# Kernel tuning notes

Measured on AMD Instinct MI355X. Metric: run time of the kernel, lower is better.

## Reference

```python
import jax, jax.numpy as jnp
import numpy as np

B, D_IN, HD, HN = 16384, 1024, 128, 8
D = HD * HN  # 1024
PROJ = int((4.0 / 3.0) * D)  # 1365
EPS = 1e-5


def setup_inputs() -> dict:
    key = jax.random.key(0)
    ks = jax.random.split(key, 16)
    s = 0.02
    inp = {
        'seq': jax.random.normal(ks[0], (B, D_IN), jnp.float32),
        'c0': jnp.zeros((B, D), jnp.float32),
        'n0': jnp.ones((B, D), jnp.float32),
        'h0': jax.random.normal(ks[1], (B, D), jnp.float32) * 0.1,
        'm0': jnp.zeros((B, D), jnp.float32),
        'ln_w': jnp.ones((D_IN,), jnp.float32),
        'ln_b': jnp.zeros((D_IN,), jnp.float32),
        'Wz': jax.random.normal(ks[2], (D, D_IN), jnp.float32) * s,
        'bz': jnp.zeros((D,), jnp.float32),
        'Wi': jax.random.normal(ks[3], (D, D_IN), jnp.float32) * s,
        'bi': jnp.zeros((D,), jnp.float32),
        'Wo': jax.random.normal(ks[4], (D, D_IN), jnp.float32) * s,
        'bo': jnp.zeros((D,), jnp.float32),
        'Wf': jax.random.normal(ks[5], (D, D_IN), jnp.float32) * s,
        'bf': jnp.zeros((D,), jnp.float32),
        'Rz': jax.random.normal(ks[6], (HN, HD, HD), jnp.float32) * s,
        'Ri': jax.random.normal(ks[7], (HN, HD, HD), jnp.float32) * s,
        'Ro': jax.random.normal(ks[8], (HN, HD, HD), jnp.float32) * s,
        'Rf': jax.random.normal(ks[9], (HN, HD, HD), jnp.float32) * s,
        'gn_w': jnp.ones((D,), jnp.float32),
        'gn_b': jnp.zeros((D,), jnp.float32),
        'up_w': jax.random.normal(ks[10], (2 * PROJ, D), jnp.float32) * s,
        'up_b': jnp.zeros((2 * PROJ,), jnp.float32),
        'down_w': jax.random.normal(ks[11], (D_IN, PROJ), jnp.float32) * s,
        'down_b': jnp.zeros((D_IN,), jnp.float32),
    }
    return inp


def _layernorm(x, w, b):
    mu = jnp.mean(x, axis=-1, keepdims=True)
    var = jnp.mean(jnp.square(x - mu), axis=-1, keepdims=True)
    return (x - mu) * jax.lax.rsqrt(var + EPS) * w + b


def _groupnorm(x, w, b):
    # x: (B, D) -> groups of HD channels per head
    xr = x.reshape(x.shape[0], HN, HD)
    mu = jnp.mean(xr, axis=-1, keepdims=True)
    var = jnp.mean(jnp.square(xr - mu), axis=-1, keepdims=True)
    xn = ((xr - mu) * jax.lax.rsqrt(var + EPS)).reshape(x.shape)
    return xn * w + b


def _block_linear(h, R):
    # block-diagonal recurrence: per-head (HD,HD) matmul
    hr = h.reshape(h.shape[0], HN, HD)
    return jnp.einsum('hed,bhd->bhe', R, hr).reshape(h.shape)


def reference(seq, c0, n0, h0, m0, ln_w, ln_b, Wz, bz, Wi, bi, Wo, bo, Wf, bf,
              Rz, Ri, Ro, Rf, gn_w, gn_b, up_w, up_b, down_w, down_b):
    x_t = _layernorm(seq, ln_w, ln_b)
    x_c = x_t  # use_conv=False default path
    i_t = x_c @ Wi.T + bi + _block_linear(h0, Ri)
    f_t = x_c @ Wf.T + bf + _block_linear(h0, Rf)
    z_t = x_t @ Wz.T + bz + _block_linear(h0, Rz)
    o_t = x_t @ Wo.T + bo + _block_linear(h0, Ro)
    m_t = jnp.maximum(f_t + m0, i_t)
    i_e = jnp.exp(i_t - m_t)
    f_e = jnp.exp(f_t - m_t + m0)
    z_a = jnp.tanh(z_t)
    o_a = jax.nn.sigmoid(o_t)
    c_t = f_e * c0 + i_e * z_a
    n_t = f_e * n0 + i_e
    h_t = o_a * (c_t / n_t)
    out = _groupnorm(h_t, gn_w, gn_b)
    up = out @ up_w.T + up_b
    out1, out2 = jnp.split(up, 2, axis=-1)
    out = out1 + jax.nn.gelu(out2, approximate=False)
    out = out @ down_w.T + down_b
    return (out + seq, c_t, n_t, h_t, m_t)
```

## Files before the change

kernel.cpp:

```cpp
#include <hip/hip_runtime.h>
#include <hip/hip_bf16.h>
#include <cstdint>
#include <type_traits>

typedef __attribute__((ext_vector_type(8))) __bf16 bf16x8;
typedef __attribute__((ext_vector_type(8))) short short8;
typedef __attribute__((ext_vector_type(4))) float f32x4;
using u16 = unsigned short;

template <typename T, typename = void> struct mfma_ok : std::false_type {};
template <typename T>
struct mfma_ok<T, std::void_t<decltype(__builtin_amdgcn_mfma_f32_16x16x32_bf16(
    std::declval<T>(), std::declval<T>(), std::declval<f32x4>(), 0, 0, 0))>>
    : std::true_type {};
using frag_t = std::conditional_t<mfma_ok<bf16x8>::value, bf16x8, short8>;
static_assert(sizeof(frag_t) == 16, "frag must be 4 VGPRs");

template <typename T>
__device__ __forceinline__ f32x4 MFMA(T a, T b, f32x4 c) {
  return __builtin_amdgcn_mfma_f32_16x16x32_bf16(a, b, c, 0, 0, 0);
}

__device__ __forceinline__ void gl_lds16(const u16* g, u16* l) {
  __builtin_amdgcn_global_load_lds(
      (const __attribute__((address_space(1))) unsigned int*)g,
      (__attribute__((address_space(3))) unsigned int*)l, 16, 0, 0);
}

__device__ __forceinline__ u16 f2bf(float v) {
  __hip_bfloat16 h = __float2bfloat16(v);
  return __builtin_bit_cast(u16, h);
}

__device__ __forceinline__ int xcd_swz(int wid, int nwg) {
  return (wid & 7) * (nwg >> 3) + (wid >> 3);
}

__device__ __forceinline__ void gemm256(
    const u16* __restrict__ A, int lda,
    const u16* __restrict__ B, int ldb, int K,
    u16* lds, f32x4 (&acc)[8][4])
{
  const int t = threadIdx.x;
  const int l = t & 63;
  const int w = t >> 6;
  const int wm = w >> 2, wc = w & 3;

  const int cs = (t & 3) ^ ((t >> 3) & 3);
  const u16* gA = A + (t >> 2) * lda + cs * 8;
  const u16* gB = B + (t >> 2) * ldb + cs * 8;

  const int lr = l & 15, lk = l >> 4;
  const int ck = (lk ^ ((lr >> 1) & 3)) * 8;
  const int ab = (wm * 128 + lr) * 32 + ck;
  const int bb = 8192 + (wc * 64 + lr) * 32 + ck;

  const int ns = K >> 5;

#define STG(s) do {                                            \
    u16* s_ = lds + ((s) & 3) * 16384;                         \
    const u16* a_ = gA + (s) * 32;                             \
    const u16* b_ = gB + (s) * 32;                             \
    gl_lds16(a_,             s_ + w * 512);                    \
    gl_lds16(a_ + 128 * lda, s_ +  4096 + w * 512);            \
    gl_lds16(b_,             s_ +  8192 + w * 512);            \
    gl_lds16(b_ + 128 * ldb, s_ + 12288 + w * 512);            \
  } while (0)

  STG(0);
  STG(1);
  asm volatile("s_waitcnt vmcnt(4)" ::: "memory");
  __builtin_amdgcn_s_barrier();

  for (int s = 0; s < ns; ++s) {
    u16* cur = lds + (s & 3) * 16384;
    if (s + 2 < ns) STG(s + 2);

    frag_t a[8], b[4];
#pragma unroll
    for (int fm = 0; fm < 8; ++fm)
      a[fm] = *(const frag_t*)(cur + ab + fm * 512);
#pragma unroll
    for (int fn = 0; fn < 4; ++fn)
      b[fn] = *(const frag_t*)(cur + bb + fn * 512);

    __builtin_amdgcn_s_setprio(1);
#pragma unroll
    for (int fn = 0; fn < 4; ++fn)
#pragma unroll
      for (int fm = 0; fm < 8; ++fm)
        acc[fm][fn] = MFMA(a[fm], b[fn], acc[fm][fn]);
    __builtin_amdgcn_s_setprio(0);

    if (s + 1 < ns) {
      if (s + 2 < ns) asm volatile("s_waitcnt vmcnt(4)" ::: "memory");
      else            asm volatile("s_waitcnt vmcnt(0)" ::: "memory");
      __builtin_amdgcn_s_barrier();
    }
  }
#undef STG
}

__global__ __launch_bounds__(256) void prep_kernel(
    const float* __restrict__ Wi, const float* __restrict__ Wf,
    const float* __restrict__ Wz, const float* __restrict__ Wo,
    const float* __restrict__ Ri, const float* __restrict__ Rf,
    const float* __restrict__ Rz, const float* __restrict__ Ro,
    const float* __restrict__ upw, const float* __restrict__ dnw,
    u16* __restrict__ Wint, u16* __restrict__ Rint,
    u16* __restrict__ upint, u16* __restrict__ dnp)
{
  const int stride = gridDim.x * 256;
  for (int i = blockIdx.x * 256 + threadIdx.x; i < 9043968; i += stride) {
    if (i < 4194304) {
      const int s = i >> 18, v = (i >> 10) & 255, k = i & 1023;
      const int wc = v >> 6, gsel = (v >> 4) & 3, c16 = v & 15;
      const int srcRow = s * 64 + wc * 16 + c16;
      const float* W = (gsel == 0) ? Wi : (gsel == 1) ? Wf : (gsel == 2) ? Wz : Wo;
      Wint[i] = f2bf(W[srcRow * 1024 + k]);
    } else if (i < 4718592) {
      const int j = i - 4194304;
      const int s = j >> 15, v = (j >> 7) & 255, k = j & 127;
      const int wc = v >> 6, gsel = (v >> 4) & 3, c16 = v & 15;
      const int head = s >> 1;
      const int colInHead = (s & 1) * 64 + wc * 16 + c16;
      const float* R = (gsel == 0) ? Ri : (gsel == 1) ? Rf : (gsel == 2) ? Rz : Ro;
      Rint[j] = f2bf(R[head * 16384 + colInHead * 128 + k]);
    } else if (i < 7602176) {
      const int j = i - 4718592;
      const int vcol = j >> 10, k = j & 1023;
      const int tile = vcol >> 8, wc = (vcol >> 6) & 3;
      const int half = (vcol >> 5) & 1, c32 = vcol & 31;
      const int a = tile * 128 + wc * 32 + c32;
      upint[j] = (a < 1365) ? f2bf(upw[(half * 1365 + a) * 1024 + k]) : (u16)0;
    } else {
      const int j = i - 7602176;
      const int row = j / 1408, k = j - row * 1408;
      dnp[j] = (k < 1365) ? f2bf(dnw[row * 1365 + k]) : (u16)0;
    }
  }
}

__global__ __launch_bounds__(256) void ln_kernel(
    const float* __restrict__ seq, const float* __restrict__ h0,
    const float* __restrict__ lnw, const float* __restrict__ lnb,
    u16* __restrict__ xb, u16* __restrict__ h0b)
{
  const int row = blockIdx.x;
  const int t = threadIdx.x;
  const float4 v = ((const float4*)(seq + (size_t)row * 1024))[t];
  float s = v.x + v.y + v.z + v.w;
  float q = v.x * v.x + v.y * v.y + v.z * v.z + v.w * v.w;
#pragma unroll
  for (int o = 32; o >= 1; o >>= 1) { s += __shfl_xor(s, o); q += __shfl_xor(q, o); }
  __shared__ float sm[8];
  const int l = t & 63, w = t >> 6;
  if (l == 0) { sm[w] = s; sm[4 + w] = q; }
  __syncthreads();
  s = sm[0] + sm[1] + sm[2] + sm[3];
  q = sm[4] + sm[5] + sm[6] + sm[7];
  const float mu = s * (1.f / 1024.f);
  const float var = q * (1.f / 1024.f) - mu * mu;
  const float rstd = rsqrtf(var + 1e-5f);
  const float4 wv = ((const float4*)lnw)[t];
  const float4 bv = ((const float4*)lnb)[t];
  ushort4 o4;
  o4.x = f2bf((v.x - mu) * rstd * wv.x + bv.x);
  o4.y = f2bf((v.y - mu) * rstd * wv.y + bv.y);
  o4.z = f2bf((v.z - mu) * rstd * wv.z + bv.z);
  o4.w = f2bf((v.w - mu) * rstd * wv.w + bv.w);
  ((ushort4*)(xb + (size_t)row * 1024))[t] = o4;
  const float4 h = ((const float4*)(h0 + (size_t)row * 1024))[t];
  ushort4 h4;
  h4.x = f2bf(h.x); h4.y = f2bf(h.y); h4.z = f2bf(h.z); h4.w = f2bf(h.w);
  ((ushort4*)(h0b + (size_t)row * 1024))[t] = h4;
}

__global__ __launch_bounds__(512, 1) void gate_kernel(
    const u16* __restrict__ xb, const u16* __restrict__ h0b,
    const u16* __restrict__ Wint, const u16* __restrict__ Rint,
    const float* __restrict__ bi, const float* __restrict__ bfv,
    const float* __restrict__ bz, const float* __restrict__ bo,
    const float* __restrict__ c0, const float* __restrict__ n0i,
    const float* __restrict__ m0,
    float* __restrict__ oc, float* __restrict__ on,
    float* __restrict__ oh, float* __restrict__ om)
{
  __shared__ __align__(16) u16 lds[65536];
  const int wid = xcd_swz(blockIdx.x, 1024);
  const int s = wid & 15;
  const int m0r = (wid >> 4) * 256;
  f32x4 acc[8][4] = {};
  gemm256(xb + (size_t)m0r * 1024, 1024, Wint + s * 262144, 1024, 1024, lds, acc);
  const int head = s >> 1;
  gemm256(h0b + (size_t)m0r * 1024 + head * 128, 1024,
          Rint + s * 32768, 128, 128, lds, acc);

  const int t = threadIdx.x, l = t & 63, w = t >> 6, wm = w >> 2, wc = w & 3;
  const int cc = s * 64 + wc * 16 + (l & 15);
  const float biv = bi[cc], bfvv = bfv[cc], bzv = bz[cc], bov = bo[cc];
#pragma unroll
  for (int fm = 0; fm < 8; ++fm) {
    const int rbase = m0r + wm * 128 + fm * 16 + (l >> 4) * 4;
#pragma unroll
    for (int r = 0; r < 4; ++r) {
      const size_t idx = (size_t)(rbase + r) * 1024 + cc;
      const float it = acc[fm][0][r] + biv;
      const float ft = acc[fm][1][r] + bfvv;
      const float zt = acc[fm][2][r] + bzv;
      const float ot = acc[fm][3][r] + bov;
      const float mp = m0[idx];
      const float mt = fmaxf(ft + mp, it);
      const float ie = __expf(it - mt);
      const float fe = __expf(ft - mt + mp);
      const float ct = fe * c0[idx] + ie * tanhf(zt);
      const float nt = fe * n0i[idx] + ie;
      const float ht = (ct / nt) / (1.f + __expf(-ot));
      oc[idx] = ct; on[idx] = nt; oh[idx] = ht; om[idx] = mt;
    }
  }
}

__global__ __launch_bounds__(256) void gn_kernel(
    const float* __restrict__ h, const float* __restrict__ gw,
    const float* __restrict__ gb, u16* __restrict__ gnb)
{
  const int t = threadIdx.x, l = t & 63, w = t >> 6;
  for (int grp = blockIdx.x * 4 + w; grp < 16384 * 8; grp += gridDim.x * 4) {
    const int b = grp >> 3, hd = grp & 7;
    const float2 v = ((const float2*)(h + b * 1024 + hd * 128))[l];
    float s = v.x + v.y, q = v.x * v.x + v.y * v.y;
#pragma unroll
    for (int o = 32; o >= 1; o >>= 1) { s += __shfl_xor(s, o); q += __shfl_xor(q, o); }
    const float mu = s * (1.f / 128.f);
    const float var = q * (1.f / 128.f) - mu * mu;
    const float rstd = rsqrtf(var + 1e-5f);
    const float2 wv = ((const float2*)(gw + hd * 128))[l];
    const float2 bv = ((const float2*)(gb + hd * 128))[l];
    ushort2 o2;
    o2.x = f2bf((v.x - mu) * rstd * wv.x + bv.x);
    o2.y = f2bf((v.y - mu) * rstd * wv.y + bv.y);
    ((ushort2*)(gnb + b * 1024 + hd * 128))[l] = o2;
  }
}

__global__ __launch_bounds__(512, 1) void up_kernel(
    const u16* __restrict__ gnb, const u16* __restrict__ upint,
    const float* __restrict__ upb, u16* __restrict__ g)
{
  __shared__ __align__(16) u16 lds[65536];
  const int wid = xcd_swz(blockIdx.x, 704);
  const int vt = wid % 11, mt = wid / 11;
  const int m0r = mt * 256;
  f32x4 acc[8][4] = {};
  gemm256(gnb + (size_t)m0r * 1024, 1024, upint + vt * 262144, 1024, 1024,
          lds, acc);
  const int t = threadIdx.x, l = t & 63, w = t >> 6, wm = w >> 2, wc = w & 3;
#pragma unroll
  for (int fm = 0; fm < 8; ++fm) {
    const int rbase = m0r + wm * 128 + fm * 16 + (l >> 4) * 4;
#pragma unroll
    for (int fn = 0; fn < 2; ++fn) {
      const int a = vt * 128 + wc * 32 + fn * 16 + (l & 15);
      const float b1 = (a < 1365) ? upb[a] : 0.f;
      const float b2 = (a < 1365) ? upb[1365 + a] : 0.f;
#pragma unroll
      for (int r = 0; r < 4; ++r) {
        const float u1 = acc[fm][fn][r] + b1;
        const float u2 = acc[fm][fn + 2][r] + b2;
        const float ge = 0.5f * u2 * (1.f + erff(u2 * 0.70710678118654752f));
        g[(size_t)(rbase + r) * 1408 + a] = f2bf(u1 + ge);
      }
    }
  }
}

__global__ __launch_bounds__(512, 1) void down_kernel(
    const u16* __restrict__ g, const u16* __restrict__ dnp,
    const float* __restrict__ dnb, const float* __restrict__ seq,
    float* __restrict__ out)
{
  __shared__ __align__(16) u16 lds[65536];
  const int wid = xcd_swz(blockIdx.x, 256);
  const int nc = (wid & 3) * 256;
  const int m0r = (wid >> 2) * 256;
  f32x4 acc[8][4] = {};
  gemm256(g + (size_t)m0r * 1408, 1408, dnp + nc * 1408, 1408, 1408, lds, acc);
  const int t = threadIdx.x, l = t & 63, w = t >> 6, wm = w >> 2, wc = w & 3;
#pragma unroll
  for (int fm = 0; fm < 8; ++fm) {
    const int rbase = m0r + wm * 128 + fm * 16 + (l >> 4) * 4;
#pragma unroll
    for (int fn = 0; fn < 4; ++fn) {
      const int cc = nc + wc * 64 + fn * 16 + (l & 15);
      const float bb = dnb[cc];
#pragma unroll
      for (int r = 0; r < 4; ++r) {
        const size_t idx = (size_t)(rbase + r) * 1024 + cc;
        out[idx] = acc[fm][fn][r] + bb + seq[idx];
      }
    }
  }
}

extern "C" void kernel_launch(void* const* d_in, const int* in_sizes, int n_in,
                              void* d_out, int out_size, void* d_ws, size_t ws_size,
                              hipStream_t stream) {
  const float* seq = (const float*)d_in[0];
  const float* c0  = (const float*)d_in[1];
  const float* n0i = (const float*)d_in[2];
  const float* h0  = (const float*)d_in[3];
  const float* m0  = (const float*)d_in[4];
  const float* lnw = (const float*)d_in[5];
  const float* lnb = (const float*)d_in[6];
  const float* Wz  = (const float*)d_in[7];
  const float* bz  = (const float*)d_in[8];
  const float* Wi  = (const float*)d_in[9];
  const float* bi  = (const float*)d_in[10];
  const float* Wo  = (const float*)d_in[11];
  const float* bo  = (const float*)d_in[12];
  const float* Wf  = (const float*)d_in[13];
  const float* bf_ = (const float*)d_in[14];
  const float* Rz  = (const float*)d_in[15];
  const float* Ri  = (const float*)d_in[16];
  const float* Ro  = (const float*)d_in[17];
  const float* Rf  = (const float*)d_in[18];
  const float* gw  = (const float*)d_in[19];
  const float* gb  = (const float*)d_in[20];
  const float* upw = (const float*)d_in[21];
  const float* upb = (const float*)d_in[22];
  const float* dnw = (const float*)d_in[23];
  const float* dnb = (const float*)d_in[24];

  char* ws = (char*)d_ws;
  u16* xb   = (u16*)(ws);
  u16* h0b  = (u16*)(ws + 33554432);
  u16* Wint = (u16*)(ws + 67108864);
  u16* Rint = (u16*)(ws + 75497472);
  u16* upc  = (u16*)(ws + 76546048);
  u16* dnp  = (u16*)(ws + 82313216);
  u16* g    = (u16*)(ws + 85196800);

  float* out = (float*)d_out;
  float* oc = out + 16777216;
  float* on = out + 2 * 16777216;
  float* oh = out + 3 * 16777216;
  float* om = out + 4 * 16777216;

  prep_kernel<<<dim3(2048), dim3(256), 0, stream>>>(
      Wi, Wf, Wz, Wo, Ri, Rf, Rz, Ro, upw, dnw, Wint, Rint, upc, dnp);
  ln_kernel<<<dim3(16384), dim3(256), 0, stream>>>(seq, h0, lnw, lnb, xb, h0b);
  gate_kernel<<<dim3(1024), dim3(512), 0, stream>>>(
      xb, h0b, Wint, Rint, bi, bf_, bz, bo, c0, n0i, m0, oc, on, oh, om);
  gn_kernel<<<dim3(2048), dim3(256), 0, stream>>>(oh, gw, gb, xb);
  up_kernel<<<dim3(704), dim3(512), 0, stream>>>(xb, upc, upb, g);
  down_kernel<<<dim3(256), dim3(512), 0, stream>>>(g, dnp, dnb, seq, out);
}
```

Before: 515.8 us.

## Restructure GEMM main loop into fine-grained interleaved load/compute schedule

The 256x256 GEMM main loop moves from a 4-stage single-k-step pipeline to a double-buffered 64-wide k-tile. Each tile is split into four quarter phases that interleave the global-to-LDS staging of the next tile, the LDS fragment reads and the MFMA groups, with a barrier after every phase. The goal is to hide LDS read latency and global loads behind MFMA issue, in the style of ping-pong scheduling. In exchange there are more barriers per iteration and more live fragment registers, and the new swizzle and wait counts must stay consistent.

Result: no change. 515.5 us (-0.1%).

```diff
diff --git a/kernel.cpp b/kernel.cpp
--- a/kernel.cpp
+++ b/kernel.cpp
@@ -36,6 +36,11 @@
   return (wid & 7) * (nwg >> 3) + (wid >> 3);
 }
 
+#define VMC(n) asm volatile("s_waitcnt vmcnt(" #n ")" ::: "memory")
+#define BARR() do { asm volatile("" ::: "memory");                        \
+    __builtin_amdgcn_s_barrier();                                         \
+    asm volatile("" ::: "memory"); } while (0)
+
 __device__ __forceinline__ void gemm256(
     const u16* __restrict__ A, int lda,
     const u16* __restrict__ B, int ldb, int K,
@@ -46,59 +51,96 @@
   const int w = t >> 6;
   const int wm = w >> 2, wc = w & 3;
 
-  const int cs = (t & 3) ^ ((t >> 3) & 3);
-  const u16* gA = A + (t >> 2) * lda + cs * 8;
-  const u16* gB = B + (t >> 2) * ldb + cs * 8;
+  const int srow = t >> 2;
+  const int cs = ((t & 3) ^ ((srow >> 1) & 3)) * 8;
 
   const int lr = l & 15, lk = l >> 4;
   const int ck = (lk ^ ((lr >> 1) & 3)) * 8;
-  const int ab = (wm * 128 + lr) * 32 + ck;
-  const int bb = 8192 + (wc * 64 + lr) * 32 + ck;
-
-  const int ns = K >> 5;
-
-#define STG(s) do {                                            \
-    u16* s_ = lds + ((s) & 3) * 16384;                         \
-    const u16* a_ = gA + (s) * 32;                             \
-    const u16* b_ = gB + (s) * 32;                             \
-    gl_lds16(a_,             s_ + w * 512);                    \
-    gl_lds16(a_ + 128 * lda, s_ +  4096 + w * 512);            \
-    gl_lds16(b_,             s_ +  8192 + w * 512);            \
-    gl_lds16(b_ + 128 * ldb, s_ + 12288 + w * 512);            \
+
+  u16* buf0 = lds;
+  u16* buf1 = lds + 32768;
+  const int nt = K >> 6;
+
+#define STAGE_U(bufp, op, kh, kt) do {                                    \
+    const u16* g0_ = (op) ? B : A;                                        \
+    const int ld_ = (op) ? ldb : lda;                                     \
+    const int kb_ = (kt) * 64 + (kh) * 32;                                \
+    gl_lds16(g0_ + srow * ld_ + kb_ + cs,                                 \
+             (bufp) + (op) * 16384 + (kh) * 8192 + w * 512);              \
+    gl_lds16(g0_ + (srow + 128) * ld_ + kb_ + cs,                         \
+             (bufp) + (op) * 16384 + (kh) * 8192 + 4096 + w * 512);       \
   } while (0)
 
-  STG(0);
-  STG(1);
-  asm volatile("s_waitcnt vmcnt(4)" ::: "memory");
-  __builtin_amdgcn_s_barrier();
-
-  for (int s = 0; s < ns; ++s) {
-    u16* cur = lds + (s & 3) * 16384;
-    if (s + 2 < ns) STG(s + 2);
-
-    frag_t a[8], b[4];
-#pragma unroll
-    for (int fm = 0; fm < 8; ++fm)
-      a[fm] = *(const frag_t*)(cur + ab + fm * 512);
-#pragma unroll
-    for (int fn = 0; fn < 4; ++fn)
-      b[fn] = *(const frag_t*)(cur + bb + fn * 512);
-
-    __builtin_amdgcn_s_setprio(1);
-#pragma unroll
-    for (int fn = 0; fn < 4; ++fn)
-#pragma unroll
-      for (int fm = 0; fm < 8; ++fm)
-        acc[fm][fn] = MFMA(a[fm], b[fn], acc[fm][fn]);
-    __builtin_amdgcn_s_setprio(0);
-
-    if (s + 1 < ns) {
-      if (s + 2 < ns) asm volatile("s_waitcnt vmcnt(4)" ::: "memory");
-      else            asm volatile("s_waitcnt vmcnt(0)" ::: "memory");
-      __builtin_amdgcn_s_barrier();
+#define RD_A(dst, bufp, kh) do {                                          \
+    _Pragma("unroll")                                                     \
+    for (int fm = 0; fm < 8; ++fm)                                        \
+      dst[fm] = *(const frag_t*)((bufp) + (kh) * 8192 +                   \
+                   (wm * 128 + fm * 16 + lr) * 32 + ck);                  \
+  } while (0)
+
+#define RD_B(dst, bufp, kh, nh) do {                                      \
+    _Pragma("unroll")                                                     \
+    for (int fn = 0; fn < 2; ++fn)                                        \
+      dst[fn] = *(const frag_t*)((bufp) + 16384 + (kh) * 8192 +           \
+                   (wc * 64 + (nh) * 32 + fn * 16 + lr) * 32 + ck);       \
+  } while (0)
+
+#define MMQ(AR, BR, n0) do {                                              \
+    __builtin_amdgcn_s_setprio(1);                                        \
+    _Pragma("unroll")                                                     \
+    for (int fn = 0; fn < 2; ++fn)                                        \
+      _Pragma("unroll")                                                   \
+      for (int fm = 0; fm < 8; ++fm)                                      \
+        acc[fm][(n0) + fn] = MFMA(AR[fm], BR[fn], acc[fm][(n0) + fn]);    \
+    __builtin_amdgcn_s_setprio(0);                                        \
+  } while (0)
+
+  frag_t Ar0[8], Ar1[8], Br00[2], Br01[2], Br10[2], Br11[2];
+
+  STAGE_U(buf0, 0, 0, 0);
+  STAGE_U(buf0, 1, 0, 0);
+  STAGE_U(buf0, 0, 1, 0);
+  STAGE_U(buf0, 1, 1, 0);
+  VMC(4);
+  BARR();
+  RD_A(Ar0, buf0, 0);
+  RD_B(Br00, buf0, 0, 0);
+
+  for (int kt = 0; kt < nt; ++kt) {
+    u16* cur = (kt & 1) ? buf1 : buf0;
+    u16* nxt = (kt & 1) ? buf0 : buf1;
+    const bool more = (kt + 1 < nt);
+
+    RD_B(Br01, cur, 0, 1);
+    if (more) STAGE_U(nxt, 0, 0, kt + 1);
+    MMQ(Ar0, Br00, 0);
+    if (more) { VMC(2); } else { VMC(0); }
+    BARR();
+
+    RD_A(Ar1, cur, 1);
+    RD_B(Br10, cur, 1, 0);
+    if (more) STAGE_U(nxt, 1, 0, kt + 1);
+    MMQ(Ar0, Br01, 2);
+    BARR();
+
+    RD_B(Br11, cur, 1, 1);
+    if (more) STAGE_U(nxt, 0, 1, kt + 1);
+    MMQ(Ar1, Br10, 0);
+    if (more) { VMC(2); }
+    BARR();
+
+    if (more) {
+      RD_A(Ar0, nxt, 0);
+      RD_B(Br00, nxt, 0, 0);
+      STAGE_U(nxt, 1, 1, kt + 1);
     }
-  }
-#undef STG
+    MMQ(Ar1, Br11, 2);
+    BARR();
+  }
+#undef STAGE_U
+#undef RD_A
+#undef RD_B
+#undef MMQ
 }
 
 __global__ __launch_bounds__(256) void prep_kernel(
```
